# Kernel tuning notes

Hardware: AMD Instinct MI355X
Metric: run time of the kernel (lower is better)

Reference implementation:

```python
import jax, jax.numpy as jnp
import numpy as np

N = 8192
D_IN = 1024
D_OUT = 1024


def setup_inputs() -> dict:
    key = jax.random.key(0)
    k0, k1, k2, k3 = jax.random.split(key, 4)
    scale = 1.0 / np.sqrt(D_IN)  # roughly matches nn.Linear init magnitude
    return {
        "x": jax.random.normal(k0, (N, D_IN), dtype=jnp.float32),
        "Wq": jax.random.normal(k1, (D_IN, D_OUT), dtype=jnp.float32) * scale,
        "Wk": jax.random.normal(k2, (D_IN, D_OUT), dtype=jnp.float32) * scale,
        "Wv": jax.random.normal(k3, (D_IN, D_OUT), dtype=jnp.float32) * scale,
    }


def reference(x, Wq, Wk, Wv):
    # QKV projections (bias-free Linear); weights stored [d_in, d_out]
    q = x @ Wq  # [N, d_out]
    k = x @ Wk  # [N, d_out]
    v = x @ Wv  # [N, d_out]
    # full N x N attention scores, scaled by sqrt(d_out), softmax over keys
    scores = jnp.einsum("nd,md->nm", q, k) / jnp.sqrt(jnp.asarray(k.shape[-1], x.dtype))
    weights = jax.nn.softmax(scores, axis=-1)
    return weights @ v  # [N, d_out]
```

## Files before the change

kernel.cpp:

```cpp
#include <hip/hip_runtime.h>
#include <hip/hip_bf16.h>
#include <stdint.h>
#include <stddef.h>

using bf16 = __hip_bfloat16;

typedef __attribute__((ext_vector_type(8))) short bf16x8;
typedef __attribute__((ext_vector_type(4))) float f32x4;

#define NROWS 8192
#define DDIM  1024

#define GLDS16(gsrc, ldst)                                                     \
  __builtin_amdgcn_global_load_lds(                                            \
      (const __attribute__((address_space(1))) uint32_t*)(gsrc),               \
      (__attribute__((address_space(3))) uint32_t*)(ldst), 16, 0, 0)

#define MFMA16(a, b, c) __builtin_amdgcn_mfma_f32_16x16x32_bf16((a), (b), (c), 0, 0, 0)

__global__ void cvt_f32_bf16_k(const float* __restrict__ in, bf16* __restrict__ out, int n) {
  int i = blockIdx.x * blockDim.x + threadIdx.x;
  int idx = i * 4;
  if (idx < n) {
    float4 v = *reinterpret_cast<const float4*>(in + idx);
    alignas(8) bf16 t[4] = {(bf16)v.x, (bf16)v.y, (bf16)v.z, (bf16)v.w};
    *reinterpret_cast<uint2*>(out + idx) = *reinterpret_cast<const uint2*>(t);
  }
}

template <typename Tin>
__global__ void transpose_bf16_k(const Tin* __restrict__ in, bf16* __restrict__ out,
                                 int R, int C, int ldin) {
  __shared__ float tile[32][33];
  int bx = blockIdx.x * 32;
  int by = blockIdx.y * 32;
  int tx = threadIdx.x, ty = threadIdx.y;
#pragma unroll
  for (int i = 0; i < 32; i += 8)
    tile[ty + i][tx] = (float)in[(size_t)(by + ty + i) * ldin + (bx + tx)];
  __syncthreads();
#pragma unroll
  for (int i = 0; i < 32; i += 8)
    out[(size_t)(bx + ty + i) * R + (by + tx)] = (bf16)tile[tx][ty + i];
}

__global__ void rowsum_k(const bf16* __restrict__ P, float* __restrict__ Z, int Kc) {
  int lane = threadIdx.x & 63;
  int wave = threadIdx.x >> 6;
  int row = blockIdx.x * 4 + wave;
  const bf16* p = P + (size_t)row * Kc;
  float s = 0.f;
  for (int c = lane * 8; c < Kc; c += 64 * 8) {
    bf16x8 v = *reinterpret_cast<const bf16x8*>(p + c);
#pragma unroll
    for (int j = 0; j < 8; j++)
      s += __uint_as_float(((uint32_t)(uint16_t)v[j]) << 16);
  }
#pragma unroll
  for (int off = 32; off > 0; off >>= 1) s += __shfl_down(s, off);
  if (lane == 0) Z[row] = s;
}

__global__ void combine_k(const float* __restrict__ P0, const float* __restrict__ P1,
                          const float* __restrict__ Z, float* __restrict__ out, int total) {
  int i = blockIdx.x * blockDim.x + threadIdx.x;
  int idx = i * 4;
  if (idx < total) {
    float4 a = *reinterpret_cast<const float4*>(P0 + idx);
    float4 b = *reinterpret_cast<const float4*>(P1 + idx);
    float rz = 1.0f / Z[idx >> 10];
    float4 o;
    o.x = (a.x + b.x) * rz; o.y = (a.y + b.y) * rz;
    o.z = (a.z + b.z) * rz; o.w = (a.w + b.w) * rz;
    *reinterpret_cast<float4*>(out + idx) = o;
  }
}

template <int EPI>
__global__ __launch_bounds__(256) void gemm_bt_k(
    const bf16* __restrict__ A, const bf16* __restrict__ B, void* __restrict__ Cv,
    int M, int N, int K, float scale) {
  __shared__ alignas(16) bf16 As[128 * 32];
  __shared__ alignas(16) bf16 Bs[128 * 32];

  const int tid = threadIdx.x;
  const int lane = tid & 63;
  const int wave = tid >> 6;
  const int wr = (wave >> 1) * 64;
  const int wc = (wave & 1) * 64;

  const int mBase = blockIdx.y * 128;
  const int nBase = blockIdx.x * 128;

  const int srow = tid >> 2;
  const int skel = (tid & 3) * 8;

  const bf16* gA0 = A + (size_t)(mBase + srow) * K + skel;
  const bf16* gA1 = A + (size_t)(mBase + srow + 64) * K + skel;
  const bf16* gB0 = B + (size_t)(nBase + srow) * K + skel;
  const bf16* gB1 = B + (size_t)(nBase + srow + 64) * K + skel;

  bf16* lA0 = &As[srow * 32 + skel];
  bf16* lA1 = &As[(srow + 64) * 32 + skel];
  bf16* lB0 = &Bs[srow * 32 + skel];
  bf16* lB1 = &Bs[(srow + 64) * 32 + skel];

  f32x4 acc[4][4];
  f32x4 zero = {0.f, 0.f, 0.f, 0.f};
#pragma unroll
  for (int i = 0; i < 4; i++)
#pragma unroll
    for (int j = 0; j < 4; j++) acc[i][j] = zero;

  const int fr = lane & 15;
  const int fk = (lane >> 4) * 8;

  for (int k0 = 0; k0 < K; k0 += 32) {
    GLDS16(gA0 + k0, lA0);
    GLDS16(gA1 + k0, lA1);
    GLDS16(gB0 + k0, lB0);
    GLDS16(gB1 + k0, lB1);
    __syncthreads();

    bf16x8 a[4], b[4];
#pragma unroll
    for (int mi = 0; mi < 4; mi++)
      a[mi] = *reinterpret_cast<const bf16x8*>(&As[(wr + mi * 16 + fr) * 32 + fk]);
#pragma unroll
    for (int nj = 0; nj < 4; nj++)
      b[nj] = *reinterpret_cast<const bf16x8*>(&Bs[(wc + nj * 16 + fr) * 32 + fk]);
#pragma unroll
    for (int mi = 0; mi < 4; mi++)
#pragma unroll
      for (int nj = 0; nj < 4; nj++)
        acc[mi][nj] = __builtin_amdgcn_mfma_f32_16x16x32_bf16(a[mi], b[nj], acc[mi][nj], 0, 0, 0);
    __syncthreads();
  }

#pragma unroll
  for (int mi = 0; mi < 4; mi++) {
#pragma unroll
    for (int nj = 0; nj < 4; nj++) {
      int col = nBase + wc + nj * 16 + fr;
#pragma unroll
      for (int j = 0; j < 4; j++) {
        int row = mBase + wr + mi * 16 + (lane >> 4) * 4 + j;
        float v = acc[mi][nj][j];
        if (EPI == 0) {
          ((bf16*)Cv)[(size_t)row * N + col] = (bf16)(v * scale);
        }
      }
    }
  }
}

template <int EPI>
__global__ __launch_bounds__(512, 2) void gemm256_k(
    const bf16* __restrict__ A, const bf16* __restrict__ B, void* __restrict__ Cv,
    int M, int N, int K, int ksplit) {
  __shared__ alignas(1024) bf16 smem[4 * 16384];

  const int tid = threadIdx.x;
  const int lane = tid & 63;
  const int wave = tid >> 6;
  const int wm = wave >> 2;
  const int wn = wave & 3;

  const int nwgx = gridDim.x;
  const int nwg = nwgx * gridDim.y;
  const int wg = blockIdx.y * nwgx + blockIdx.x;
  const int cpx = nwg >> 3;
  const int swz = (wg & 7) * cpx + (wg >> 3);
  const int bx = swz % nwgx;
  const int by = swz / nwgx;
  const int mBase = by * 256;
  const int nBase = bx * 256;

  const int z = blockIdx.z;
  const int kbase = z * ksplit;
  const int NT = ksplit / 32;

  const int sr = lane >> 2;
  const int ssl = (lane & 3) ^ ((lane >> 3) & 3);
  const bf16* srcA0 = A + (size_t)(mBase + wave * 16 + sr) * K + kbase + ssl * 8;
  const bf16* srcA1 = A + (size_t)(mBase + (wave + 8) * 16 + sr) * K + kbase + ssl * 8;
  const bf16* srcB0 = B + (size_t)(nBase + wave * 16 + sr) * K + kbase + ssl * 8;
  const bf16* srcB1 = B + (size_t)(nBase + (wave + 8) * 16 + sr) * K + kbase + ssl * 8;

  const int fr = lane & 15;
  const int laneElem = fr * 32 + (((lane >> 4) ^ ((fr >> 1) & 3)) * 8);

  f32x4 acc[8][4];
  f32x4 zero = {0.f, 0.f, 0.f, 0.f};
#pragma unroll
  for (int m = 0; m < 8; m++)
#pragma unroll
    for (int n = 0; n < 4; n++) acc[m][n] = zero;

  auto stageH0 = [&](int t) {
    bf16* base = smem + (t & 3) * 16384;
    int kk = t * 32;
    GLDS16(srcA0 + kk, base + wave * 512);
    GLDS16(srcA1 + kk, base + (wave + 8) * 512);
  };
  auto stageH1 = [&](int t) {
    bf16* base = smem + (t & 3) * 16384;
    int kk = t * 32;
    GLDS16(srcB0 + kk, base + 8192 + wave * 512);
    GLDS16(srcB1 + kk, base + 8192 + (wave + 8) * 512);
  };
  auto rdA = [&](const bf16* buf, int m) {
    return *reinterpret_cast<const bf16x8*>(buf + (wm * 128 + m * 16) * 32 + laneElem);
  };
  auto rdB = [&](const bf16* buf, int n) {
    return *reinterpret_cast<const bf16x8*>(buf + 8192 + (wn * 64 + n * 16) * 32 + laneElem);
  };

#define PHASE_SYNC()                                                           \
  __builtin_amdgcn_s_barrier();                                                \
  asm volatile("s_waitcnt lgkmcnt(0)" ::: "memory");                           \
  __builtin_amdgcn_sched_barrier(0)

  stageH0(0); stageH1(0);
  stageH0(1); stageH1(1);
  stageH0(2); stageH1(2);
  asm volatile("s_waitcnt vmcnt(8)" ::: "memory");
  __builtin_amdgcn_s_barrier();

  for (int t = 0; t < NT; ++t) {
    const bf16* buf = smem + (t & 3) * 16384;
    const bool st = (t + 3 < NT);
    bf16x8 bfr[4], afr[4];

#pragma unroll
    for (int n = 0; n < 4; n++) bfr[n] = rdB(buf, n);
#pragma unroll
    for (int m = 0; m < 4; m++) afr[m] = rdA(buf, m);
    if (st) stageH0(t + 3);
    PHASE_SYNC();
    __builtin_amdgcn_s_setprio(1);
#pragma unroll
    for (int m = 0; m < 4; m++)
#pragma unroll
      for (int n = 0; n < 4; n++)
        acc[m][n] = MFMA16(afr[m], bfr[n], acc[m][n]);
    __builtin_amdgcn_s_setprio(0);
    __builtin_amdgcn_s_barrier();

#pragma unroll
    for (int m = 0; m < 4; m++) afr[m] = rdA(buf, m + 4);
    if (st) stageH1(t + 3);
    if (t + 1 < NT) {
      int hi = (t + 3 < NT) ? (t + 3) : (NT - 1);
      int slack = hi - (t + 1);
      if (slack >= 2)      asm volatile("s_waitcnt vmcnt(8)" ::: "memory");
      else if (slack == 1) asm volatile("s_waitcnt vmcnt(4)" ::: "memory");
      else                 asm volatile("s_waitcnt vmcnt(0)" ::: "memory");
    }
    PHASE_SYNC();
    __builtin_amdgcn_s_setprio(1);
#pragma unroll
    for (int m = 0; m < 4; m++)
#pragma unroll
      for (int n = 0; n < 4; n++)
        acc[m + 4][n] = MFMA16(afr[m], bfr[n], acc[m + 4][n]);
    __builtin_amdgcn_s_setprio(0);
    __builtin_amdgcn_s_barrier();
  }
#undef PHASE_SYNC

#pragma unroll
  for (int m = 0; m < 8; m++) {
#pragma unroll
    for (int n = 0; n < 4; n++) {
      int col = nBase + wn * 64 + n * 16 + fr;
#pragma unroll
      for (int j = 0; j < 4; j++) {
        int row = mBase + wm * 128 + m * 16 + (lane >> 4) * 4 + j;
        float v = acc[m][n][j];
        if (EPI == 1) {
          ((bf16*)Cv)[(size_t)row * N + col] = (bf16)__expf(v);
        } else {
          float* Cp = (float*)Cv + (size_t)z * M * N;
          Cp[(size_t)row * N + col] = v;
        }
      }
    }
  }
}

extern "C" void kernel_launch(void* const* d_in, const int* in_sizes, int n_in,
                              void* d_out, int out_size, void* d_ws, size_t ws_size,
                              hipStream_t stream) {
  (void)in_sizes; (void)n_in; (void)out_size; (void)ws_size;
  const float* x  = (const float*)d_in[0];
  const float* Wq = (const float*)d_in[1];
  const float* Wk = (const float*)d_in[2];
  const float* Wv = (const float*)d_in[3];
  float* out = (float*)d_out;

  char* ws = (char*)d_ws;
  size_t o = 0;
  float* Z   = (float*)(ws + o); o += 64 * 1024;
  size_t xb_off = o;
  bf16* xb  = (bf16*)(ws + o); o += (size_t)NROWS * DDIM * 2;
  bf16* WqT = (bf16*)(ws + o); o += (size_t)DDIM * DDIM * 2;
  bf16* WkT = (bf16*)(ws + o); o += (size_t)DDIM * DDIM * 2;
  bf16* WvT = (bf16*)(ws + o); o += (size_t)DDIM * DDIM * 2;
  bf16* Qb  = (bf16*)(ws + o); o += (size_t)NROWS * DDIM * 2;
  bf16* Kb  = (bf16*)(ws + o); o += (size_t)NROWS * DDIM * 2;
  bf16* Vsp = (bf16*)(ws + o); o += (size_t)NROWS * DDIM * 2;
  bf16* Vt  = (bf16*)(ws + o); o += (size_t)DDIM * NROWS * 2;
  bf16* P   = (bf16*)(ws + o); o += (size_t)NROWS * NROWS * 2;
  float* Pp = (float*)(ws + xb_off);
  (void)Vsp;

  {
    int n = NROWS * DDIM;
    cvt_f32_bf16_k<<<(n / 4 + 255) / 256, 256, 0, stream>>>(x, xb, n);
  }
  {
    dim3 tb(32, 8);
    transpose_bf16_k<float><<<dim3(32, 32), tb, 0, stream>>>(Wq, WqT, DDIM, DDIM, DDIM);
    transpose_bf16_k<float><<<dim3(32, 32), tb, 0, stream>>>(Wk, WkT, DDIM, DDIM, DDIM);
    transpose_bf16_k<float><<<dim3(32, 32), tb, 0, stream>>>(Wv, WvT, DDIM, DDIM, DDIM);
  }
  {
    dim3 grid(DDIM / 128, NROWS / 128);
    gemm_bt_k<0><<<grid, 256, 0, stream>>>(xb, WqT, Qb, NROWS, DDIM, DDIM, 0.03125f);
    gemm_bt_k<0><<<grid, 256, 0, stream>>>(xb, WkT, Kb, NROWS, DDIM, DDIM, 1.0f);
    gemm_bt_k<0><<<dim3(NROWS / 128, DDIM / 128), 256, 0, stream>>>(
        WvT, xb, Vt, DDIM, NROWS, DDIM, 1.0f);
  }
  gemm256_k<1><<<dim3(NROWS / 256, NROWS / 256, 1), 512, 0, stream>>>(
      Qb, Kb, P, NROWS, NROWS, DDIM, DDIM);
  rowsum_k<<<NROWS / 4, 256, 0, stream>>>(P, Z, NROWS);
  gemm256_k<3><<<dim3(DDIM / 256, NROWS / 256, 2), 512, 0, stream>>>(
      P, Vt, Pp, NROWS, DDIM, NROWS, NROWS / 2);
  {
    int total = NROWS * DDIM;
    combine_k<<<(total / 4 + 255) / 256, 256, 0, stream>>>(
        Pp, Pp + (size_t)NROWS * DDIM, Z, out, total);
  }
}
```

Before: 418.5 us.

## Fuse QKV projections into one large-tile GEMM with split-layout epilogue

Replaces the three separate 128x128-tile projection GEMMs with a single 256x256-tile GEMM over concatenated transposed weights. A new epilogue scatters columns into separate Q, K and V buffers and applies the Q scale. V is then transposed with a bf16 transpose kernel instead of being computed directly in transposed form. This aims to use the more efficient pipelined GEMM and cut launches, but it adds an extra transpose pass over V.

```diff
diff --git a/kernel.cpp b/kernel.cpp
--- a/kernel.cpp
+++ b/kernel.cpp
@@ -77,84 +77,6 @@
 }
 
 template <int EPI>
-__global__ __launch_bounds__(256) void gemm_bt_k(
-    const bf16* __restrict__ A, const bf16* __restrict__ B, void* __restrict__ Cv,
-    int M, int N, int K, float scale) {
-  __shared__ alignas(16) bf16 As[128 * 32];
-  __shared__ alignas(16) bf16 Bs[128 * 32];
-
-  const int tid = threadIdx.x;
-  const int lane = tid & 63;
-  const int wave = tid >> 6;
-  const int wr = (wave >> 1) * 64;
-  const int wc = (wave & 1) * 64;
-
-  const int mBase = blockIdx.y * 128;
-  const int nBase = blockIdx.x * 128;
-
-  const int srow = tid >> 2;
-  const int skel = (tid & 3) * 8;
-
-  const bf16* gA0 = A + (size_t)(mBase + srow) * K + skel;
-  const bf16* gA1 = A + (size_t)(mBase + srow + 64) * K + skel;
-  const bf16* gB0 = B + (size_t)(nBase + srow) * K + skel;
-  const bf16* gB1 = B + (size_t)(nBase + srow + 64) * K + skel;
-
-  bf16* lA0 = &As[srow * 32 + skel];
-  bf16* lA1 = &As[(srow + 64) * 32 + skel];
-  bf16* lB0 = &Bs[srow * 32 + skel];
-  bf16* lB1 = &Bs[(srow + 64) * 32 + skel];
-
-  f32x4 acc[4][4];
-  f32x4 zero = {0.f, 0.f, 0.f, 0.f};
-#pragma unroll
-  for (int i = 0; i < 4; i++)
-#pragma unroll
-    for (int j = 0; j < 4; j++) acc[i][j] = zero;
-
-  const int fr = lane & 15;
-  const int fk = (lane >> 4) * 8;
-
-  for (int k0 = 0; k0 < K; k0 += 32) {
-    GLDS16(gA0 + k0, lA0);
-    GLDS16(gA1 + k0, lA1);
-    GLDS16(gB0 + k0, lB0);
-    GLDS16(gB1 + k0, lB1);
-    __syncthreads();
-
-    bf16x8 a[4], b[4];
-#pragma unroll
-    for (int mi = 0; mi < 4; mi++)
-      a[mi] = *reinterpret_cast<const bf16x8*>(&As[(wr + mi * 16 + fr) * 32 + fk]);
-#pragma unroll
-    for (int nj = 0; nj < 4; nj++)
-      b[nj] = *reinterpret_cast<const bf16x8*>(&Bs[(wc + nj * 16 + fr) * 32 + fk]);
-#pragma unroll
-    for (int mi = 0; mi < 4; mi++)
-#pragma unroll
-      for (int nj = 0; nj < 4; nj++)
-        acc[mi][nj] = __builtin_amdgcn_mfma_f32_16x16x32_bf16(a[mi], b[nj], acc[mi][nj], 0, 0, 0);
-    __syncthreads();
-  }
-
-#pragma unroll
-  for (int mi = 0; mi < 4; mi++) {
-#pragma unroll
-    for (int nj = 0; nj < 4; nj++) {
-      int col = nBase + wc + nj * 16 + fr;
-#pragma unroll
-      for (int j = 0; j < 4; j++) {
-        int row = mBase + wr + mi * 16 + (lane >> 4) * 4 + j;
-        float v = acc[mi][nj][j];
-        if (EPI == 0) {
-          ((bf16*)Cv)[(size_t)row * N + col] = (bf16)(v * scale);
-        }
-      }
-    }
-  }
-}
-
-template <int EPI>
 __global__ __launch_bounds__(512, 2) void gemm256_k(
     const bf16* __restrict__ A, const bf16* __restrict__ B, void* __restrict__ Cv,
     int M, int N, int K, int ksplit) {
@@ -280,6 +202,11 @@
         float v = acc[m][n][j];
         if (EPI == 1) {
           ((bf16*)Cv)[(size_t)row * N + col] = (bf16)__expf(v);
+        } else if (EPI == 4) {
+          int mi2 = col >> 10;
+          float sc = (mi2 == 0) ? 0.03125f : 1.0f;
+          ((bf16*)Cv)[(size_t)mi2 * M * 1024 + (size_t)row * 1024 + (col & 1023)] =
+              (bf16)(v * sc);
         } else {
           float* Cp = (float*)Cv + (size_t)z * M * N;
           Cp[(size_t)row * N + col] = v;
@@ -301,19 +228,18 @@
 
   char* ws = (char*)d_ws;
   size_t o = 0;
-  float* Z   = (float*)(ws + o); o += 64 * 1024;
+  float* Z     = (float*)(ws + o); o += 64 * 1024;
   size_t xb_off = o;
-  bf16* xb  = (bf16*)(ws + o); o += (size_t)NROWS * DDIM * 2;
-  bf16* WqT = (bf16*)(ws + o); o += (size_t)DDIM * DDIM * 2;
-  bf16* WkT = (bf16*)(ws + o); o += (size_t)DDIM * DDIM * 2;
-  bf16* WvT = (bf16*)(ws + o); o += (size_t)DDIM * DDIM * 2;
-  bf16* Qb  = (bf16*)(ws + o); o += (size_t)NROWS * DDIM * 2;
-  bf16* Kb  = (bf16*)(ws + o); o += (size_t)NROWS * DDIM * 2;
-  bf16* Vsp = (bf16*)(ws + o); o += (size_t)NROWS * DDIM * 2;
-  bf16* Vt  = (bf16*)(ws + o); o += (size_t)DDIM * NROWS * 2;
-  bf16* P   = (bf16*)(ws + o); o += (size_t)NROWS * NROWS * 2;
-  float* Pp = (float*)(ws + xb_off);
-  (void)Vsp;
+  bf16* xb     = (bf16*)(ws + o); o += (size_t)NROWS * DDIM * 2;
+  bf16* WqkvT  = (bf16*)(ws + o); o += (size_t)3 * DDIM * DDIM * 2;
+  bf16* QKV    = (bf16*)(ws + o); o += (size_t)3 * NROWS * DDIM * 2;
+  bf16* Vt     = (bf16*)(ws + o); o += (size_t)DDIM * NROWS * 2;
+  bf16* P      = (bf16*)(ws + o); o += (size_t)NROWS * NROWS * 2;
+  float* Pp    = (float*)(ws + xb_off);
+
+  bf16* Qb = QKV;
+  bf16* Kb = QKV + (size_t)NROWS * DDIM;
+  bf16* Vb = QKV + (size_t)2 * NROWS * DDIM;
 
   {
     int n = NROWS * DDIM;
@@ -321,16 +247,16 @@
   }
   {
     dim3 tb(32, 8);
-    transpose_bf16_k<float><<<dim3(32, 32), tb, 0, stream>>>(Wq, WqT, DDIM, DDIM, DDIM);
-    transpose_bf16_k<float><<<dim3(32, 32), tb, 0, stream>>>(Wk, WkT, DDIM, DDIM, DDIM);
-    transpose_bf16_k<float><<<dim3(32, 32), tb, 0, stream>>>(Wv, WvT, DDIM, DDIM, DDIM);
-  }
-  {
-    dim3 grid(DDIM / 128, NROWS / 128);
-    gemm_bt_k<0><<<grid, 256, 0, stream>>>(xb, WqT, Qb, NROWS, DDIM, DDIM, 0.03125f);
-    gemm_bt_k<0><<<grid, 256, 0, stream>>>(xb, WkT, Kb, NROWS, DDIM, DDIM, 1.0f);
-    gemm_bt_k<0><<<dim3(NROWS / 128, DDIM / 128), 256, 0, stream>>>(
-        WvT, xb, Vt, DDIM, NROWS, DDIM, 1.0f);
+    transpose_bf16_k<float><<<dim3(32, 32), tb, 0, stream>>>(Wq, WqkvT,               DDIM, DDIM, DDIM);
+    transpose_bf16_k<float><<<dim3(32, 32), tb, 0, stream>>>(Wk, WqkvT + 1024 * 1024, DDIM, DDIM, DDIM);
+    transpose_bf16_k<float><<<dim3(32, 32), tb, 0, stream>>>(Wv, WqkvT + 2048 * 1024, DDIM, DDIM, DDIM);
+  }
+  gemm256_k<4><<<dim3(3 * DDIM / 256, NROWS / 256, 1), 512, 0, stream>>>(
+      xb, WqkvT, QKV, NROWS, 3 * DDIM, DDIM, DDIM);
+  {
+    dim3 tb(32, 8);
+    transpose_bf16_k<bf16><<<dim3(DDIM / 32, NROWS / 32), tb, 0, stream>>>(
+        Vb, Vt, NROWS, DDIM, DDIM);
   }
   gemm256_k<1><<<dim3(NROWS / 256, NROWS / 256, 1), 512, 0, stream>>>(
       Qb, Kb, P, NROWS, NROWS, DDIM, DDIM);
```

After: 404.9 us (median of 3 runs). 1.03x faster.
